# Performance work log

Measured on AMD Instinct MI355X. Metric: run time of the kernel, lower is better.

The kernel has to match this reference:

```python
import jax, jax.numpy as jnp
import numpy as np


def setup_inputs() -> dict:
    key = jax.random.key(0)
    k1, k2 = jax.random.split(key)
    from_points = jax.random.normal(k1, (16384, 64), dtype=jnp.float32)
    to_points = jax.random.normal(k2, (16384, 64), dtype=jnp.float32)
    return {"from_points": from_points, "to_points": to_points}


def reference(from_points, to_points):
    # Squared L2 distance matrix [N, M] via ||a||^2 + ||b||^2 - 2 a.b,
    # avoiding the O(N*M*D) broadcasted intermediate of the original.
    a_sq = jnp.sum(from_points * from_points, axis=-1)          # [N]
    b_sq = jnp.sum(to_points * to_points, axis=-1)              # [M]
    cross = jnp.einsum('nd,md->nm', from_points, to_points)     # [N, M]
    dist_mat = a_sq[:, None] + b_sq[None, :] - 2.0 * cross      # [N, M]
    # Row-wise min (nearest neighbor squared distance), then sum.
    return jnp.sum(jnp.min(dist_mat, axis=1))
```

## Files before the change

kernel.cpp:

```cpp
#include <hip/hip_runtime.h>
#include <stdint.h>

#define N_PTS 16384
#define TSPLITS 32
#define TO_TILES 16
#define FGPB 16
#define NBLOCKS (TSPLITS * (256 / FGPB))

typedef __attribute__((ext_vector_type(4)))  int i32x4;
typedef __attribute__((ext_vector_type(16))) int i32x16;

__device__ __forceinline__ int imin(int a, int b) { return a < b ? a : b; }
__device__ __forceinline__ int itree16(i32x16 a) {
    int m0 = imin(imin(a[0],  a[1]),  a[2]);
    int m1 = imin(imin(a[3],  a[4]),  a[5]);
    int m2 = imin(imin(a[6],  a[7]),  a[8]);
    int m3 = imin(imin(a[9],  a[10]), a[11]);
    int m4 = imin(imin(a[12], a[13]), a[14]);
    int m5 = imin(imin(a[15], m0), m1);
    return imin(imin(imin(m2, m3), m4), m5);
}
__device__ __forceinline__ int q8(float x) {
    int q = __float2int_rn(x);
    return q < -127 ? -127 : (q > 127 ? 127 : q);
}

__global__ __launch_bounds__(256) void prep_kernel(
        const float* __restrict__ from_pts, const float* __restrict__ to_pts,
        float* __restrict__ a_sq, int* __restrict__ bsqi,
        char* __restrict__ BfQ, char* __restrict__ AtoQ,
        int* __restrict__ pmin16, float* __restrict__ out) {
    int gid = blockIdx.x * 256 + threadIdx.x;
    if (gid < N_PTS) pmin16[gid] = 0x7FFFFFFF;
    int row = gid >> 3;
    int sub = gid & 7;
    bool isFrom = row < N_PTS;
    int r = row & (N_PTS - 1);
    const float* src = isFrom ? from_pts : to_pts;
    float4 v0 = ((const float4*)src)[r * 16 + sub * 2];
    float4 v1 = ((const float4*)src)[r * 16 + sub * 2 + 1];
    float s = v0.x*v0.x + v0.y*v0.y + v0.z*v0.z + v0.w*v0.w
            + v1.x*v1.x + v1.y*v1.y + v1.z*v1.z + v1.w*v1.w;
    s += __shfl_xor(s, 1); s += __shfl_xor(s, 2); s += __shfl_xor(s, 4);
    float sc = isFrom ? -16.0f : 16.0f;
    int q0 = q8(v0.x*sc), q1 = q8(v0.y*sc), q2 = q8(v0.z*sc), q3 = q8(v0.w*sc);
    int q4 = q8(v1.x*sc), q5 = q8(v1.y*sc), q6 = q8(v1.z*sc), q7 = q8(v1.w*sc);
    int2 w;
    w.x = (q0 & 255) | ((q1 & 255) << 8) | ((q2 & 255) << 16) | (q3 << 24);
    w.y = (q4 & 255) | ((q5 & 255) << 8) | ((q6 & 255) << 16) | (q7 << 24);
    int st = r >> 5;
    int m  = r & 31;
    int kb = sub >> 2, h = (sub >> 1) & 1, half8 = sub & 1;
    size_t off = (((size_t)st * 2 + kb) * 64 + h * 32 + m) * 16 + 8 * half8;
    if (isFrom) {
        *(int2*)(BfQ + off) = w;
        if (sub == 0) a_sq[r] = s;
    } else {
        *(int2*)(AtoQ + off) = w;
        if (sub == 0)
            bsqi[st * 32 + ((m >> 2) & 1) * 16 + (m & 3) + 4 * (m >> 3)] =
                __float2int_rn(128.0f * s);
    }
    if (gid == 0) out[0] = 0.0f;
}

__global__ __launch_bounds__(512, 4) void main_kernel(
        const char* __restrict__ BfQ, const char* __restrict__ AtoQ,
        const int* __restrict__ bsqi, int* __restrict__ pmin16) {
    __shared__ __align__(16) char abuf[32768 + 2048];

    const int tid = threadIdx.x;
    const int lane = tid & 63;
    const int l31 = lane & 31;
    const int h   = lane >> 5;
    const int wv  = tid >> 6;
    const int ts  = blockIdx.x >> 4;
    const int bg  = blockIdx.x & 15;
    const int gtb = ts * TO_TILES;

    #pragma unroll
    for (int j2 = 0; j2 < 4; j2++) {
        int j = wv * 4 + j2;
        const char* g = AtoQ +
            (((size_t)(gtb + (j >> 1)) * 2 + (j & 1)) * 64 + lane) * 16;
        char* l = &abuf[j * 1024];
        __builtin_amdgcn_global_load_lds(
            (const __attribute__((address_space(1))) unsigned int*)g,
            (__attribute__((address_space(3))) unsigned int*)l, 16, 0, 0);
    }
    if (wv == 0) {
        #pragma unroll
        for (int j = 0; j < 2; j++) {
            const int* g = bsqi + gtb * 32 + j * 256 + lane * 4;
            char* l = &abuf[32768 + j * 1024];
            __builtin_amdgcn_global_load_lds(
                (const __attribute__((address_space(1))) unsigned int*)g,
                (__attribute__((address_space(3))) unsigned int*)l, 16, 0, 0);
        }
    }
    __syncthreads();

    const int fgA = bg * FGPB + wv;
    const int fgB = fgA + 8;
    i32x4 B00[2], B01[2], B10[2], B11[2];
    #pragma unroll
    for (int kb = 0; kb < 2; kb++) {
        B00[kb] = *(const i32x4*)(BfQ + (((size_t)(2 * fgA)     * 2 + kb) * 64 + lane) * 16);
        B01[kb] = *(const i32x4*)(BfQ + (((size_t)(2 * fgA + 1) * 2 + kb) * 64 + lane) * 16);
        B10[kb] = *(const i32x4*)(BfQ + (((size_t)(2 * fgB)     * 2 + kb) * 64 + lane) * 16);
        B11[kb] = *(const i32x4*)(BfQ + (((size_t)(2 * fgB + 1) * 2 + kb) * 64 + lane) * 16);
    }
    int rmin00 = 0x7FFFFFFF, rmin01 = 0x7FFFFFFF;
    int rmin10 = 0x7FFFFFFF, rmin11 = 0x7FFFFFFF;

    const int toff = wv * 2;
    #define LOADT(T, A, CU)                                                     \
        {                                                                       \
            int t_ = (T) & (TO_TILES - 1);                                      \
            A[0] = *(const i32x4*)&abuf[((t_ * 2 + 0) * 64 + lane) * 16];       \
            A[1] = *(const i32x4*)&abuf[((t_ * 2 + 1) * 64 + lane) * 16];       \
            const char* cb_ = &abuf[32768 + t_ * 128 + h * 64];                 \
            union { i32x4 f[4]; i32x16 v; } cu_;                                \
            cu_.f[0] = *(const i32x4*)(cb_ + 0);                                \
            cu_.f[1] = *(const i32x4*)(cb_ + 16);                               \
            cu_.f[2] = *(const i32x4*)(cb_ + 32);                               \
            cu_.f[3] = *(const i32x4*)(cb_ + 48);                               \
            CU = cu_.v;                                                         \
        }
    #define DOT(A, CU)                                                          \
        {                                                                       \
            __builtin_amdgcn_s_setprio(1);                                      \
            i32x16 c0 = __builtin_amdgcn_mfma_i32_32x32x32_i8(A[0], B00[0], CU, 0, 0, 0); \
            i32x16 c1 = __builtin_amdgcn_mfma_i32_32x32x32_i8(A[0], B01[0], CU, 0, 0, 0); \
            c0 = __builtin_amdgcn_mfma_i32_32x32x32_i8(A[1], B00[1], c0, 0, 0, 0); \
            c1 = __builtin_amdgcn_mfma_i32_32x32x32_i8(A[1], B01[1], c1, 0, 0, 0); \
            rmin00 = imin(rmin00, itree16(c0));                                 \
            rmin01 = imin(rmin01, itree16(c1));                                 \
            i32x16 c2 = __builtin_amdgcn_mfma_i32_32x32x32_i8(A[0], B10[0], CU, 0, 0, 0); \
            i32x16 c3 = __builtin_amdgcn_mfma_i32_32x32x32_i8(A[0], B11[0], CU, 0, 0, 0); \
            c2 = __builtin_amdgcn_mfma_i32_32x32x32_i8(A[1], B10[1], c2, 0, 0, 0); \
            c3 = __builtin_amdgcn_mfma_i32_32x32x32_i8(A[1], B11[1], c3, 0, 0, 0); \
            __builtin_amdgcn_s_setprio(0);                                      \
            rmin10 = imin(rmin10, itree16(c2));                                 \
            rmin11 = imin(rmin11, itree16(c3));                                 \
        }

    i32x4 Aa[2], Ab[2];
    i32x16 cua, cub;
    LOADT(toff, Aa, cua)
    #pragma unroll 1
    for (int t = 0; t < TO_TILES; t += 2) {
        LOADT(toff + t + 1, Ab, cub)
        DOT(Aa, cua)
        LOADT(toff + t + 2, Aa, cua)
        DOT(Ab, cub)
    }

    rmin00 = imin(rmin00, __shfl_xor(rmin00, 32));
    rmin01 = imin(rmin01, __shfl_xor(rmin01, 32));
    rmin10 = imin(rmin10, __shfl_xor(rmin10, 32));
    rmin11 = imin(rmin11, __shfl_xor(rmin11, 32));
    if (lane < 32) {
        atomicMin(&pmin16[fgA * 64 + l31],      rmin00);
        atomicMin(&pmin16[fgA * 64 + 32 + l31], rmin01);
        atomicMin(&pmin16[fgB * 64 + l31],      rmin10);
        atomicMin(&pmin16[fgB * 64 + 32 + l31], rmin11);
    }
}

__global__ __launch_bounds__(256) void finish_kernel(
        const float* __restrict__ a_sq, const int* __restrict__ pmin16,
        float* __restrict__ out) {
    int r = blockIdx.x * 256 + threadIdx.x;
    float v = a_sq[r] + (float)pmin16[r] * 0.0078125f;
    #pragma unroll
    for (int k = 1; k < 64; k <<= 1) v += __shfl_xor(v, k);
    __shared__ float red[4];
    if ((threadIdx.x & 63) == 0) red[threadIdx.x >> 6] = v;
    __syncthreads();
    if (threadIdx.x == 0)
        atomicAdd(out, red[0] + red[1] + red[2] + red[3]);
}

extern "C" void kernel_launch(void* const* d_in, const int* in_sizes, int n_in,
                              void* d_out, int out_size, void* d_ws, size_t ws_size,
                              hipStream_t stream) {
    const float* from_pts = (const float*)d_in[0];
    const float* to_pts   = (const float*)d_in[1];
    char* ws = (char*)d_ws;
    float* a_sq   = (float*)ws;
    int*   bsqi   = (int*)(ws + (64 << 10));
    int*   pmin16 = (int*)(ws + (128 << 10));
    char*  BfQ    = ws + (256 << 10);
    char*  AtoQ   = ws + (256 << 10) + (1 << 20);

    prep_kernel<<<(2 * N_PTS * 8) / 256, 256, 0, stream>>>(
        from_pts, to_pts, a_sq, bsqi, BfQ, AtoQ, pmin16, (float*)d_out);
    main_kernel<<<NBLOCKS, 512, 0, stream>>>(BfQ, AtoQ, bsqi, pmin16);
    finish_kernel<<<N_PTS / 256, 256, 0, stream>>>(a_sq, pmin16, (float*)d_out);
}
```

Measured before the change: 75.00 us.

## Switch distance MFMA from 32x32x32 to 16x16x64 int8 tiles with new layout

Replaces the 32x32x32 int8 MFMA tiling with 16x16x64 int8 MFMAs, so the full 64-dim K fits in one instruction per tile. The quantized point layout and the b-squared bias layout in the prep kernel are rewritten to match 16-row tiles. Each wave now holds 8 from-tiles in registers and accumulates 4-element outputs. This shortens the per-output min reduction tree and cuts accumulator register pressure. In exchange it issues more, smaller MFMAs and adds an extra cross-lane shuffle stage in the final reduction.

```diff
diff --git a/kernel.cpp b/kernel.cpp
--- a/kernel.cpp
+++ b/kernel.cpp
@@ -3,23 +3,12 @@
 
 #define N_PTS 16384
 #define TSPLITS 32
-#define TO_TILES 16
-#define FGPB 16
-#define NBLOCKS (TSPLITS * (256 / FGPB))
+#define TO_TILES 32
+#define NBLOCKS (TSPLITS * 16)
 
 typedef __attribute__((ext_vector_type(4)))  int i32x4;
-typedef __attribute__((ext_vector_type(16))) int i32x16;
 
 __device__ __forceinline__ int imin(int a, int b) { return a < b ? a : b; }
-__device__ __forceinline__ int itree16(i32x16 a) {
-    int m0 = imin(imin(a[0],  a[1]),  a[2]);
-    int m1 = imin(imin(a[3],  a[4]),  a[5]);
-    int m2 = imin(imin(a[6],  a[7]),  a[8]);
-    int m3 = imin(imin(a[9],  a[10]), a[11]);
-    int m4 = imin(imin(a[12], a[13]), a[14]);
-    int m5 = imin(imin(a[15], m0), m1);
-    return imin(imin(imin(m2, m3), m4), m5);
-}
 __device__ __forceinline__ int q8(float x) {
     int q = __float2int_rn(x);
     return q < -127 ? -127 : (q > 127 ? 127 : q);
@@ -48,18 +37,16 @@
     int2 w;
     w.x = (q0 & 255) | ((q1 & 255) << 8) | ((q2 & 255) << 16) | (q3 << 24);
     w.y = (q4 & 255) | ((q5 & 255) << 8) | ((q6 & 255) << 16) | (q7 << 24);
-    int st = r >> 5;
-    int m  = r & 31;
-    int kb = sub >> 2, h = (sub >> 1) & 1, half8 = sub & 1;
-    size_t off = (((size_t)st * 2 + kb) * 64 + h * 32 + m) * 16 + 8 * half8;
+    int t16 = r >> 4;
+    int m16 = r & 15;
+    int kch = sub >> 1;
+    size_t off = (size_t)t16 * 1024 + (size_t)(kch * 16 + m16) * 16 + (sub & 1) * 8;
     if (isFrom) {
         *(int2*)(BfQ + off) = w;
         if (sub == 0) a_sq[r] = s;
     } else {
         *(int2*)(AtoQ + off) = w;
-        if (sub == 0)
-            bsqi[st * 32 + ((m >> 2) & 1) * 16 + (m & 3) + 4 * (m >> 3)] =
-                __float2int_rn(128.0f * s);
+        if (sub == 0) bsqi[r] = __float2int_rn(128.0f * s);
     }
     if (gid == 0) out[0] = 0.0f;
 }
@@ -71,8 +58,7 @@
 
     const int tid = threadIdx.x;
     const int lane = tid & 63;
-    const int l31 = lane & 31;
-    const int h   = lane >> 5;
+    const int l15 = lane & 15;
     const int wv  = tid >> 6;
     const int ts  = blockIdx.x >> 4;
     const int bg  = blockIdx.x & 15;
@@ -81,8 +67,7 @@
     #pragma unroll
     for (int j2 = 0; j2 < 4; j2++) {
         int j = wv * 4 + j2;
-        const char* g = AtoQ +
-            (((size_t)(gtb + (j >> 1)) * 2 + (j & 1)) * 64 + lane) * 16;
+        const char* g = AtoQ + (size_t)(gtb + j) * 1024 + lane * 16;
         char* l = &abuf[j * 1024];
         __builtin_amdgcn_global_load_lds(
             (const __attribute__((address_space(1))) unsigned int*)g,
@@ -91,7 +76,7 @@
     if (wv == 0) {
         #pragma unroll
         for (int j = 0; j < 2; j++) {
-            const int* g = bsqi + gtb * 32 + j * 256 + lane * 4;
+            const int* g = bsqi + ts * 512 + j * 256 + lane * 4;
             char* l = &abuf[32768 + j * 1024];
             __builtin_amdgcn_global_load_lds(
                 (const __attribute__((address_space(1))) unsigned int*)g,
@@ -100,53 +85,50 @@
     }
     __syncthreads();
 
-    const int fgA = bg * FGPB + wv;
-    const int fgB = fgA + 8;
-    i32x4 B00[2], B01[2], B10[2], B11[2];
-    #pragma unroll
-    for (int kb = 0; kb < 2; kb++) {
-        B00[kb] = *(const i32x4*)(BfQ + (((size_t)(2 * fgA)     * 2 + kb) * 64 + lane) * 16);
-        B01[kb] = *(const i32x4*)(BfQ + (((size_t)(2 * fgA + 1) * 2 + kb) * 64 + lane) * 16);
-        B10[kb] = *(const i32x4*)(BfQ + (((size_t)(2 * fgB)     * 2 + kb) * 64 + lane) * 16);
-        B11[kb] = *(const i32x4*)(BfQ + (((size_t)(2 * fgB + 1) * 2 + kb) * 64 + lane) * 16);
-    }
-    int rmin00 = 0x7FFFFFFF, rmin01 = 0x7FFFFFFF;
-    int rmin10 = 0x7FFFFFFF, rmin11 = 0x7FFFFFFF;
+    const int ctb = bg * 64 + wv * 8;
+    i32x4 Bf0 = *(const i32x4*)(BfQ + (size_t)(ctb + 0) * 1024 + lane * 16);
+    i32x4 Bf1 = *(const i32x4*)(BfQ + (size_t)(ctb + 1) * 1024 + lane * 16);
+    i32x4 Bf2 = *(const i32x4*)(BfQ + (size_t)(ctb + 2) * 1024 + lane * 16);
+    i32x4 Bf3 = *(const i32x4*)(BfQ + (size_t)(ctb + 3) * 1024 + lane * 16);
+    i32x4 Bf4 = *(const i32x4*)(BfQ + (size_t)(ctb + 4) * 1024 + lane * 16);
+    i32x4 Bf5 = *(const i32x4*)(BfQ + (size_t)(ctb + 5) * 1024 + lane * 16);
+    i32x4 Bf6 = *(const i32x4*)(BfQ + (size_t)(ctb + 6) * 1024 + lane * 16);
+    i32x4 Bf7 = *(const i32x4*)(BfQ + (size_t)(ctb + 7) * 1024 + lane * 16);
 
-    const int toff = wv * 2;
+    int rmin0 = 0x7FFFFFFF, rmin1 = 0x7FFFFFFF, rmin2 = 0x7FFFFFFF,
+        rmin3 = 0x7FFFFFFF, rmin4 = 0x7FFFFFFF, rmin5 = 0x7FFFFFFF,
+        rmin6 = 0x7FFFFFFF, rmin7 = 0x7FFFFFFF;
+
+    const int cuo = (lane >> 4) * 16;
+
+    const int toff = wv * 4;
     #define LOADT(T, A, CU)                                                     \
         {                                                                       \
             int t_ = (T) & (TO_TILES - 1);                                      \
-            A[0] = *(const i32x4*)&abuf[((t_ * 2 + 0) * 64 + lane) * 16];       \
-            A[1] = *(const i32x4*)&abuf[((t_ * 2 + 1) * 64 + lane) * 16];       \
-            const char* cb_ = &abuf[32768 + t_ * 128 + h * 64];                 \
-            union { i32x4 f[4]; i32x16 v; } cu_;                                \
-            cu_.f[0] = *(const i32x4*)(cb_ + 0);                                \
-            cu_.f[1] = *(const i32x4*)(cb_ + 16);                               \
-            cu_.f[2] = *(const i32x4*)(cb_ + 32);                               \
-            cu_.f[3] = *(const i32x4*)(cb_ + 48);                               \
-            CU = cu_.v;                                                         \
+            A  = *(const i32x4*)&abuf[t_ * 1024 + lane * 16];                   \
+            CU = *(const i32x4*)&abuf[32768 + t_ * 64 + cuo];                   \
         }
+    #define TREE4(AC, RM)                                                       \
+        { RM = imin(RM, imin(imin(AC[0], AC[1]), imin(AC[2], AC[3]))); }
     #define DOT(A, CU)                                                          \
         {                                                                       \
             __builtin_amdgcn_s_setprio(1);                                      \
-            i32x16 c0 = __builtin_amdgcn_mfma_i32_32x32x32_i8(A[0], B00[0], CU, 0, 0, 0); \
-            i32x16 c1 = __builtin_amdgcn_mfma_i32_32x32x32_i8(A[0], B01[0], CU, 0, 0, 0); \
-            c0 = __builtin_amdgcn_mfma_i32_32x32x32_i8(A[1], B00[1], c0, 0, 0, 0); \
-            c1 = __builtin_amdgcn_mfma_i32_32x32x32_i8(A[1], B01[1], c1, 0, 0, 0); \
-            rmin00 = imin(rmin00, itree16(c0));                                 \
-            rmin01 = imin(rmin01, itree16(c1));                                 \
-            i32x16 c2 = __builtin_amdgcn_mfma_i32_32x32x32_i8(A[0], B10[0], CU, 0, 0, 0); \
-            i32x16 c3 = __builtin_amdgcn_mfma_i32_32x32x32_i8(A[0], B11[0], CU, 0, 0, 0); \
-            c2 = __builtin_amdgcn_mfma_i32_32x32x32_i8(A[1], B10[1], c2, 0, 0, 0); \
-            c3 = __builtin_amdgcn_mfma_i32_32x32x32_i8(A[1], B11[1], c3, 0, 0, 0); \
+            i32x4 a0 = __builtin_amdgcn_mfma_i32_16x16x64_i8(A, Bf0, CU, 0, 0, 0); \
+            i32x4 a1 = __builtin_amdgcn_mfma_i32_16x16x64_i8(A, Bf1, CU, 0, 0, 0); \
+            i32x4 a2 = __builtin_amdgcn_mfma_i32_16x16x64_i8(A, Bf2, CU, 0, 0, 0); \
+            i32x4 a3 = __builtin_amdgcn_mfma_i32_16x16x64_i8(A, Bf3, CU, 0, 0, 0); \
+            i32x4 a4 = __builtin_amdgcn_mfma_i32_16x16x64_i8(A, Bf4, CU, 0, 0, 0); \
+            i32x4 a5 = __builtin_amdgcn_mfma_i32_16x16x64_i8(A, Bf5, CU, 0, 0, 0); \
+            i32x4 a6 = __builtin_amdgcn_mfma_i32_16x16x64_i8(A, Bf6, CU, 0, 0, 0); \
+            i32x4 a7 = __builtin_amdgcn_mfma_i32_16x16x64_i8(A, Bf7, CU, 0, 0, 0); \
             __builtin_amdgcn_s_setprio(0);                                      \
-            rmin10 = imin(rmin10, itree16(c2));                                 \
-            rmin11 = imin(rmin11, itree16(c3));                                 \
+            TREE4(a0, rmin0); TREE4(a1, rmin1);                                 \
+            TREE4(a2, rmin2); TREE4(a3, rmin3);                                 \
+            TREE4(a4, rmin4); TREE4(a5, rmin5);                                 \
+            TREE4(a6, rmin6); TREE4(a7, rmin7);                                 \
         }
 
-    i32x4 Aa[2], Ab[2];
-    i32x16 cua, cub;
+    i32x4 Aa, Ab, cua, cub;
     LOADT(toff, Aa, cua)
     #pragma unroll 1
     for (int t = 0; t < TO_TILES; t += 2) {
@@ -156,15 +138,20 @@
         DOT(Ab, cub)
     }
 
-    rmin00 = imin(rmin00, __shfl_xor(rmin00, 32));
-    rmin01 = imin(rmin01, __shfl_xor(rmin01, 32));
-    rmin10 = imin(rmin10, __shfl_xor(rmin10, 32));
-    rmin11 = imin(rmin11, __shfl_xor(rmin11, 32));
-    if (lane < 32) {
-        atomicMin(&pmin16[fgA * 64 + l31],      rmin00);
-        atomicMin(&pmin16[fgA * 64 + 32 + l31], rmin01);
-        atomicMin(&pmin16[fgB * 64 + l31],      rmin10);
-        atomicMin(&pmin16[fgB * 64 + 32 + l31], rmin11);
+    #define REDC(RM) RM = imin(RM, __shfl_xor(RM, 16)); \
+                     RM = imin(RM, __shfl_xor(RM, 32));
+    REDC(rmin0) REDC(rmin1) REDC(rmin2) REDC(rmin3)
+    REDC(rmin4) REDC(rmin5) REDC(rmin6) REDC(rmin7)
+    if (lane < 16) {
+        int cb = bg * 1024 + wv * 128 + l15;
+        atomicMin(&pmin16[cb +   0], rmin0);
+        atomicMin(&pmin16[cb +  16], rmin1);
+        atomicMin(&pmin16[cb +  32], rmin2);
+        atomicMin(&pmin16[cb +  48], rmin3);
+        atomicMin(&pmin16[cb +  64], rmin4);
+        atomicMin(&pmin16[cb +  80], rmin5);
+        atomicMin(&pmin16[cb +  96], rmin6);
+        atomicMin(&pmin16[cb + 112], rmin7);
     }
 }
 
```

Measured after the change: 77.14 us. 2.9% more time.
